# Optimization experiments

Measured on AMD Instinct MI355X. Metric: run time of the kernel, lower is better.

## Reference

```python
import jax, jax.numpy as jnp
import numpy as np

VOCAB_SIZE = 250002
UNUSED_TOKEN_IDS = np.array([0, 2, 1, 3])  # cls, eos, pad, unk (XLM-R tokenizer)
EPS = 1e-12


def _l2norm(x):
    n = jnp.sqrt(jnp.sum(x * x, axis=-1, keepdims=True))
    return x / jnp.maximum(n, EPS)


def setup_inputs() -> dict:
    key = jax.random.key(0)
    k1, k2, k3, k4 = jax.random.split(key, 4)
    B, S, H = 16, 2048, 1024
    hidden_state = jax.random.normal(k1, (B, S, H), dtype=jnp.float32)
    attention_mask = jnp.ones((B, S), dtype=jnp.float32)
    input_ids = jax.random.randint(k2, (B, S), 0, VOCAB_SIZE, dtype=jnp.int64)
    sparse_W = jax.random.normal(k3, (H, 1), dtype=jnp.float32) * 0.02
    sparse_b = jnp.zeros((1,), dtype=jnp.float32)
    colbert_W = jax.random.normal(k4, (H, H), dtype=jnp.float32) * 0.02
    colbert_b = jnp.zeros((H,), dtype=jnp.float32)
    return {
        "hidden_state": hidden_state,
        "attention_mask": attention_mask,
        "input_ids": input_ids,
        "sparse_W": sparse_W,
        "sparse_b": sparse_b,
        "colbert_W": colbert_W,
        "colbert_b": colbert_b,
    }


def reference(hidden_state, attention_mask, input_ids, sparse_W, sparse_b, colbert_W, colbert_b):
    B, S, H = hidden_state.shape
    # dense vector: CLS token, L2-normalized
    dense_vecs = _l2norm(hidden_state[:, 0])  # (B, H)

    # sparse: relu(Linear(H,1)) per token, scatter into vocab, max over seq.
    # scatter into zeros(B,S,V) + max over dim=1 == per-batch scatter-max into (B,V)
    token_weights = jax.nn.relu(
        jnp.einsum("bsh,ho->bso", hidden_state, sparse_W) + sparse_b
    )[..., 0]  # (B, S)
    batch_idx = jnp.arange(B)[:, None]  # (B, 1)
    sparse_vecs = jnp.zeros((B, VOCAB_SIZE), dtype=token_weights.dtype)
    sparse_vecs = sparse_vecs.at[batch_idx, input_ids].max(token_weights)
    # zero out special tokens (cls/eos/pad/unk)
    sparse_vecs = sparse_vecs.at[:, jnp.asarray(UNUSED_TOKEN_IDS)].set(0.0)

    # colbert: Linear(H,H) on tokens 1:, masked, then L2-normalized
    colbert_vecs = jnp.einsum("bsh,hd->bsd", hidden_state[:, 1:], colbert_W) + colbert_b
    colbert_vecs = colbert_vecs * attention_mask[:, 1:, None]
    colbert_vecs = _l2norm(colbert_vecs)  # (B, S-1, H)

    return dense_vecs, sparse_vecs, colbert_vecs
```

## Files before the change

### kernel.cpp

```cpp
#include <hip/hip_runtime.h>
#include <hip/hip_bf16.h>

#define HDIM 1024
#define SEQ  2048
#define BATCH 16
#define VOCAB 250002
#define M_TOT (BATCH * SEQ)
#define DENSE_OFF 0
#define SPARSE_OFF (BATCH * HDIM)
#define COLBERT_OFF (SPARSE_OFF + BATCH * VOCAB)
#define COLBERT_ROWS (BATCH * (SEQ - 1))

typedef __attribute__((ext_vector_type(8))) short short8;
typedef __attribute__((ext_vector_type(4))) float f32x4;

static __device__ __forceinline__ unsigned short f2bf(float f) {
  union { float f; unsigned u; } v; v.f = f;
  unsigned r = v.u + 0x7fffu + ((v.u >> 16) & 1u);
  return (unsigned short)(r >> 16);
}

__global__ __launch_bounds__(256) void cast_sparse_kernel(
    const float* __restrict__ hidden,
    const float* __restrict__ sparse_W,
    const float* __restrict__ sparse_b,
    const int* __restrict__ input_ids,
    unsigned short* __restrict__ hidden_bf,
    float* __restrict__ sparse_out)
{
  const int token = blockIdx.x * 4 + (threadIdx.x >> 6);
  const int lane = threadIdx.x & 63;

  const float4* xr = (const float4*)(hidden + (size_t)token * HDIM);
  const float4* wr = (const float4*)sparse_W;
  ushort4* hb = (ushort4*)(hidden_bf + (size_t)token * HDIM);

  float dot = 0.0f;
#pragma unroll
  for (int i = 0; i < 4; i++) {
    const int idx = i * 64 + lane;
    float4 xv = xr[idx];
    float4 wv = wr[idx];
    dot = fmaf(xv.x, wv.x, dot);
    dot = fmaf(xv.y, wv.y, dot);
    dot = fmaf(xv.z, wv.z, dot);
    dot = fmaf(xv.w, wv.w, dot);
    ushort4 o;
    o.x = f2bf(xv.x); o.y = f2bf(xv.y); o.z = f2bf(xv.z); o.w = f2bf(xv.w);
    hb[idx] = o;
  }
#pragma unroll
  for (int off = 32; off; off >>= 1) dot += __shfl_down(dot, off);

  if (lane == 0) {
    float w = dot + sparse_b[0];
    if (w > 0.0f) {
      int id = input_ids[token];
      if (id > 3) {
        int b = token >> 11;
        atomicMax((int*)(sparse_out + (size_t)b * VOCAB + id), __float_as_int(w));
      }
    }
  }
}

__global__ __launch_bounds__(256) void dense_kernel(
    const float* __restrict__ hidden, float* __restrict__ out)
{
  const int b = blockIdx.x;
  const int t = threadIdx.x;
  const float4* x = (const float4*)(hidden + (size_t)b * SEQ * HDIM);
  float4 v = x[t];
  float ss = v.x * v.x + v.y * v.y + v.z * v.z + v.w * v.w;
#pragma unroll
  for (int off = 32; off; off >>= 1) ss += __shfl_down(ss, off);
  __shared__ float red[4];
  if ((t & 63) == 0) red[t >> 6] = ss;
  __syncthreads();
  float tot = red[0] + red[1] + red[2] + red[3];
  float inv = 1.0f / fmaxf(sqrtf(tot), 1e-12f);
  v.x *= inv; v.y *= inv; v.z *= inv; v.w *= inv;
  ((float4*)(out + (size_t)b * HDIM))[t] = v;
}

__global__ __launch_bounds__(256) void transpose_w_kernel(
    const float* __restrict__ W, unsigned short* __restrict__ Wt)
{
  __shared__ float tile[32][33];
  const int n0 = blockIdx.x * 32, k0 = blockIdx.y * 32;
  const int tx = threadIdx.x, ty = threadIdx.y;
#pragma unroll
  for (int i = ty; i < 32; i += 8)
    tile[i][tx] = W[(size_t)(k0 + i) * HDIM + n0 + tx];
  __syncthreads();
#pragma unroll
  for (int i = ty; i < 32; i += 8)
    Wt[(size_t)(n0 + i) * HDIM + k0 + tx] = f2bf(tile[tx][i]);
}

__global__ __launch_bounds__(256) void gemm_colbert_kernel(
    const unsigned short* __restrict__ Abf,
    const unsigned short* __restrict__ Btbf,
    const float* __restrict__ bias,
    float* __restrict__ out)
{
  __shared__ __attribute__((aligned(16))) unsigned short As[128 * 32];
  __shared__ __attribute__((aligned(16))) unsigned short Bs[128 * 32];

  const int t = threadIdx.x;
  const int wv = t >> 6, l = t & 63;

  const int xcd = blockIdx.x & 7;
  const int local = blockIdx.x >> 3;
  const int mt = xcd * 32 + (local >> 3);
  const int nt = local & 7;
  const int mBase = mt * 128, nBase = nt * 128;
  const int wm = wv >> 1, wn = wv & 1;
  const int q = l >> 4, ml = l & 15;

  f32x4 acc[4][4] = {};

  const int c0 = t;
  const int c1 = t + 256;
  const int r0 = c0 >> 2, r1 = c1 >> 2;
  const size_t ga0 = (size_t)r0 * HDIM + (((c0 & 3) - (r0 >> 1)) & 3) * 8;
  const size_t ga1 = (size_t)r1 * HDIM + (((c1 & 3) - (r1 >> 1)) & 3) * 8;

  const unsigned short* Ab = Abf + (size_t)mBase * HDIM;
  const unsigned short* Bb = Btbf + (size_t)nBase * HDIM;

  for (int k0 = 0; k0 < HDIM; k0 += 32) {
    __builtin_amdgcn_global_load_lds(
        (const __attribute__((address_space(1))) unsigned int*)(Ab + k0 + ga0),
        (__attribute__((address_space(3))) unsigned int*)(As + wv * 512), 16, 0, 0);
    __builtin_amdgcn_global_load_lds(
        (const __attribute__((address_space(1))) unsigned int*)(Ab + k0 + ga1),
        (__attribute__((address_space(3))) unsigned int*)(As + 2048 + wv * 512), 16, 0, 0);
    __builtin_amdgcn_global_load_lds(
        (const __attribute__((address_space(1))) unsigned int*)(Bb + k0 + ga0),
        (__attribute__((address_space(3))) unsigned int*)(Bs + wv * 512), 16, 0, 0);
    __builtin_amdgcn_global_load_lds(
        (const __attribute__((address_space(1))) unsigned int*)(Bb + k0 + ga1),
        (__attribute__((address_space(3))) unsigned int*)(Bs + 2048 + wv * 512), 16, 0, 0);
    __syncthreads();

    short8 af[4], bf[4];
#pragma unroll
    for (int i = 0; i < 4; i++) {
      const int ar = wm * 64 + i * 16 + ml;
      const int br = wn * 64 + i * 16 + ml;
      af[i] = *(const short8*)(As + ar * 32 + (((q + (ar >> 1)) & 3) * 8));
      bf[i] = *(const short8*)(Bs + br * 32 + (((q + (br >> 1)) & 3) * 8));
    }
#pragma unroll
    for (int i = 0; i < 4; i++)
#pragma unroll
      for (int j = 0; j < 4; j++)
        acc[i][j] = __builtin_amdgcn_mfma_f32_16x16x32_bf16(af[i], bf[j], acc[i][j], 0, 0, 0);
    __syncthreads();
  }

#pragma unroll
  for (int j = 0; j < 4; j++) {
    const int gn = nBase + wn * 64 + j * 16 + ml;
    const float bv = bias[gn];
#pragma unroll
    for (int i = 0; i < 4; i++) {
#pragma unroll
      for (int r = 0; r < 4; r++) {
        const int gm = mBase + wm * 64 + i * 16 + q * 4 + r;
        const int s = gm & (SEQ - 1);
        if (s != 0) {
          const int b = gm >> 11;
          out[COLBERT_OFF + (size_t)(b * (SEQ - 1) + s - 1) * HDIM + gn] =
              acc[i][j][r] + bv;
        }
      }
    }
  }
}

__global__ __launch_bounds__(256) void colbert_norm_kernel(
    float* __restrict__ out, const float* __restrict__ mask)
{
  const int row = blockIdx.x * 4 + (threadIdx.x >> 6);
  const int lane = threadIdx.x & 63;
  const int b = row / (SEQ - 1);
  const int s = row - b * (SEQ - 1) + 1;
  const float mval = mask[b * SEQ + s];

  float4* p = (float4*)(out + COLBERT_OFF + (size_t)row * HDIM);
  float4 v[4];
  float ss = 0.0f;
#pragma unroll
  for (int i = 0; i < 4; i++) {
    v[i] = p[i * 64 + lane];
    ss += v[i].x * v[i].x + v[i].y * v[i].y + v[i].z * v[i].z + v[i].w * v[i].w;
  }
#pragma unroll
  for (int off = 32; off; off >>= 1) ss += __shfl_xor(ss, off);
  const float inv = mval / fmaxf(fabsf(mval) * sqrtf(ss), 1e-12f);
#pragma unroll
  for (int i = 0; i < 4; i++) {
    v[i].x *= inv; v[i].y *= inv; v[i].z *= inv; v[i].w *= inv;
    p[i * 64 + lane] = v[i];
  }
}

extern "C" void kernel_launch(void* const* d_in, const int* in_sizes, int n_in,
                              void* d_out, int out_size, void* d_ws, size_t ws_size,
                              hipStream_t stream) {
  (void)in_sizes; (void)n_in; (void)out_size; (void)ws_size;
  const float* hidden = (const float*)d_in[0];
  const float* attn_mask = (const float*)d_in[1];
  const int* input_ids = (const int*)d_in[2];
  const float* sparse_W = (const float*)d_in[3];
  const float* sparse_b = (const float*)d_in[4];
  const float* colbert_W = (const float*)d_in[5];
  const float* colbert_b = (const float*)d_in[6];
  float* out = (float*)d_out;

  unsigned short* hidden_bf = (unsigned short*)d_ws;
  unsigned short* Wt = (unsigned short*)((char*)d_ws + (size_t)M_TOT * HDIM * 2);

  hipMemsetAsync(out + SPARSE_OFF, 0, (size_t)BATCH * VOCAB * sizeof(float), stream);

  cast_sparse_kernel<<<M_TOT / 4, 256, 0, stream>>>(
      hidden, sparse_W, sparse_b, input_ids, hidden_bf, out + SPARSE_OFF);
  transpose_w_kernel<<<dim3(32, 32), dim3(32, 8), 0, stream>>>(colbert_W, Wt);
  dense_kernel<<<BATCH, 256, 0, stream>>>(hidden, out);
  gemm_colbert_kernel<<<(M_TOT / 128) * (HDIM / 128), 256, 0, stream>>>(
      hidden_bf, Wt, colbert_b, out);
  colbert_norm_kernel<<<COLBERT_ROWS / 4, 256, 0, stream>>>(out, attn_mask);
}
```

Measured before the change: 382.5 us.

## Fuse ColBERT L2 norm into GEMM epilogue and merge prep kernels

The GEMM is restructured so each 512-thread block computes 64 full rows across all 1024 output columns. It double-buffers the whole B panel in LDS and computes the row L2 norm, mask and bias in the epilogue before a single write. This removes the separate read-modify-write pass of the colbert output. The memset, the W transpose/cast and the dense CLS normalization are merged into one prep kernel to cut launch count. The cost is a very large dynamic LDS footprint (about 136 KB), which limits occupancy to one block per CU, and every block rereads the full W panel from cache.

Result: no change. 375.6 us (-1.8%).

```diff
diff --git a/kernel.cpp b/kernel.cpp
--- a/kernel.cpp
+++ b/kernel.cpp
@@ -6,10 +6,8 @@
 #define BATCH 16
 #define VOCAB 250002
 #define M_TOT (BATCH * SEQ)
-#define DENSE_OFF 0
 #define SPARSE_OFF (BATCH * HDIM)
 #define COLBERT_OFF (SPARSE_OFF + BATCH * VOCAB)
-#define COLBERT_ROWS (BATCH * (SEQ - 1))
 
 typedef __attribute__((ext_vector_type(8))) short short8;
 typedef __attribute__((ext_vector_type(4))) float f32x4;
@@ -18,6 +16,52 @@
   union { float f; unsigned u; } v; v.f = f;
   unsigned r = v.u + 0x7fffu + ((v.u >> 16) & 1u);
   return (unsigned short)(r >> 16);
+}
+
+static __device__ __forceinline__ void gll16(const unsigned short* g, unsigned short* l) {
+  __builtin_amdgcn_global_load_lds(
+      (const __attribute__((address_space(1))) unsigned int*)g,
+      (__attribute__((address_space(3))) unsigned int*)l, 16, 0, 0);
+}
+
+__global__ __launch_bounds__(256) void prep_kernel(
+    const float* __restrict__ W, unsigned short* __restrict__ Wt,
+    float* __restrict__ out, const float* __restrict__ hidden)
+{
+  __shared__ float tile[32][33];
+  __shared__ float red[4];
+  const int blk = blockIdx.x;
+  if (blk < 1024) {
+    const int n0 = (blk & 31) * 32, k0 = (blk >> 5) * 32;
+    const int tx = threadIdx.x & 31, ty = threadIdx.x >> 5;
+#pragma unroll
+    for (int i = ty; i < 32; i += 8)
+      tile[i][tx] = W[(size_t)(k0 + i) * HDIM + n0 + tx];
+    __syncthreads();
+#pragma unroll
+    for (int i = ty; i < 32; i += 8)
+      Wt[(size_t)(n0 + i) * HDIM + k0 + tx] = f2bf(tile[tx][i]);
+  } else if (blk < 1536) {
+    float4 z = {0.f, 0.f, 0.f, 0.f};
+    float4* p = (float4*)(out + SPARSE_OFF);
+    int idx = (blk - 1024) * 256 + threadIdx.x;
+#pragma unroll 1
+    for (; idx < 1000008; idx += 512 * 256) p[idx] = z;
+  } else {
+    const int b = blk - 1536;
+    const int t = threadIdx.x;
+    const float4* x = (const float4*)(hidden + (size_t)b * SEQ * HDIM);
+    float4 v = x[t];
+    float ss = v.x * v.x + v.y * v.y + v.z * v.z + v.w * v.w;
+#pragma unroll
+    for (int off = 32; off; off >>= 1) ss += __shfl_down(ss, off);
+    if ((t & 63) == 0) red[t >> 6] = ss;
+    __syncthreads();
+    float tot = red[0] + red[1] + red[2] + red[3];
+    float inv = 1.0f / fmaxf(sqrtf(tot), 1e-12f);
+    v.x *= inv; v.y *= inv; v.z *= inv; v.w *= inv;
+    ((float4*)(out + (size_t)b * HDIM))[t] = v;
+  }
 }
 
 __global__ __launch_bounds__(256) void cast_sparse_kernel(
@@ -64,146 +108,144 @@
   }
 }
 
-__global__ __launch_bounds__(256) void dense_kernel(
-    const float* __restrict__ hidden, float* __restrict__ out)
-{
-  const int b = blockIdx.x;
-  const int t = threadIdx.x;
-  const float4* x = (const float4*)(hidden + (size_t)b * SEQ * HDIM);
-  float4 v = x[t];
-  float ss = v.x * v.x + v.y * v.y + v.z * v.z + v.w * v.w;
-#pragma unroll
-  for (int off = 32; off; off >>= 1) ss += __shfl_down(ss, off);
-  __shared__ float red[4];
-  if ((t & 63) == 0) red[t >> 6] = ss;
-  __syncthreads();
-  float tot = red[0] + red[1] + red[2] + red[3];
-  float inv = 1.0f / fmaxf(sqrtf(tot), 1e-12f);
-  v.x *= inv; v.y *= inv; v.z *= inv; v.w *= inv;
-  ((float4*)(out + (size_t)b * HDIM))[t] = v;
-}
-
-__global__ __launch_bounds__(256) void transpose_w_kernel(
-    const float* __restrict__ W, unsigned short* __restrict__ Wt)
-{
-  __shared__ float tile[32][33];
-  const int n0 = blockIdx.x * 32, k0 = blockIdx.y * 32;
-  const int tx = threadIdx.x, ty = threadIdx.y;
-#pragma unroll
-  for (int i = ty; i < 32; i += 8)
-    tile[i][tx] = W[(size_t)(k0 + i) * HDIM + n0 + tx];
-  __syncthreads();
-#pragma unroll
-  for (int i = ty; i < 32; i += 8)
-    Wt[(size_t)(n0 + i) * HDIM + k0 + tx] = f2bf(tile[tx][i]);
-}
-
-__global__ __launch_bounds__(256) void gemm_colbert_kernel(
+#define BS_ELEMS (1024 * 32)
+#define AS_ELEMS (64 * 32)
+#define LDS_BYTES ((2 * BS_ELEMS + 2 * AS_ELEMS) * 2)
+
+__global__ __launch_bounds__(512, 2) void gemm_norm_kernel(
     const unsigned short* __restrict__ Abf,
     const unsigned short* __restrict__ Btbf,
     const float* __restrict__ bias,
+    const float* __restrict__ mask,
     float* __restrict__ out)
 {
-  __shared__ __attribute__((aligned(16))) unsigned short As[128 * 32];
-  __shared__ __attribute__((aligned(16))) unsigned short Bs[128 * 32];
+  extern __shared__ __align__(16) char smem[];
+  unsigned short* Bs0 = (unsigned short*)smem;
+  unsigned short* Bs1 = Bs0 + BS_ELEMS;
+  unsigned short* As0 = Bs1 + BS_ELEMS;
+  unsigned short* As1 = As0 + AS_ELEMS;
+  float* redLDS = (float*)smem;
+  float* invLDS = (float*)smem + 64 * 8;
 
   const int t = threadIdx.x;
   const int wv = t >> 6, l = t & 63;
-
-  const int xcd = blockIdx.x & 7;
-  const int local = blockIdx.x >> 3;
-  const int mt = xcd * 32 + (local >> 3);
-  const int nt = local & 7;
-  const int mBase = mt * 128, nBase = nt * 128;
-  const int wm = wv >> 1, wn = wv & 1;
   const int q = l >> 4, ml = l & 15;
-
-  f32x4 acc[4][4] = {};
-
-  const int c0 = t;
-  const int c1 = t + 256;
-  const int r0 = c0 >> 2, r1 = c1 >> 2;
-  const size_t ga0 = (size_t)r0 * HDIM + (((c0 & 3) - (r0 >> 1)) & 3) * 8;
-  const size_t ga1 = (size_t)r1 * HDIM + (((c1 & 3) - (r1 >> 1)) & 3) * 8;
-
-  const unsigned short* Ab = Abf + (size_t)mBase * HDIM;
-  const unsigned short* Bb = Btbf + (size_t)nBase * HDIM;
-
-  for (int k0 = 0; k0 < HDIM; k0 += 32) {
-    __builtin_amdgcn_global_load_lds(
-        (const __attribute__((address_space(1))) unsigned int*)(Ab + k0 + ga0),
-        (__attribute__((address_space(3))) unsigned int*)(As + wv * 512), 16, 0, 0);
-    __builtin_amdgcn_global_load_lds(
-        (const __attribute__((address_space(1))) unsigned int*)(Ab + k0 + ga1),
-        (__attribute__((address_space(3))) unsigned int*)(As + 2048 + wv * 512), 16, 0, 0);
-    __builtin_amdgcn_global_load_lds(
-        (const __attribute__((address_space(1))) unsigned int*)(Bb + k0 + ga0),
-        (__attribute__((address_space(3))) unsigned int*)(Bs + wv * 512), 16, 0, 0);
-    __builtin_amdgcn_global_load_lds(
-        (const __attribute__((address_space(1))) unsigned int*)(Bb + k0 + ga1),
-        (__attribute__((address_space(3))) unsigned int*)(Bs + 2048 + wv * 512), 16, 0, 0);
+  const int mBase = blockIdx.x * 64;
+
+  int boff[8];
+#pragma unroll
+  for (int c = 0; c < 8; c++) {
+    int cb = c * 512 + wv * 64 + l;
+    int n = cb >> 2;
+    int kc = ((cb & 3) - (n >> 1)) & 3;
+    boff[c] = n * HDIM + kc * 8;
+  }
+  int aoff;
+  {
+    int ca = wv * 64 + l;
+    int row = ca >> 2;
+    int kc = ((ca & 3) - (row >> 1)) & 3;
+    aoff = (mBase + row) * HDIM + kc * 8;
+  }
+
+  f32x4 acc[4][8] = {};
+
+#define STAGE(K0, BD, AD)                                               \
+  do {                                                                  \
+    _Pragma("unroll")                                                   \
+    for (int c = 0; c < 8; c++)                                         \
+      gll16(Btbf + boff[c] + (K0), (BD) + (c * 512 + wv * 64) * 8);     \
+    if (wv < 4) gll16(Abf + aoff + (K0), (AD) + (wv * 64) * 8);         \
+  } while (0)
+
+  STAGE(0, Bs0, As0);
+  __syncthreads();
+
+  for (int kk = 0; kk < 32; kk++) {
+    unsigned short* Bc = (kk & 1) ? Bs1 : Bs0;
+    unsigned short* Ac = (kk & 1) ? As1 : As0;
+    if (kk < 31) {
+      unsigned short* Bn = (kk & 1) ? Bs0 : Bs1;
+      unsigned short* An = (kk & 1) ? As0 : As1;
+      STAGE((kk + 1) * 32, Bn, An);
+    }
+
+    short8 af[4], bf[4];
+#pragma unroll
+    for (int i = 0; i < 4; i++) {
+      const int ar = i * 16 + ml;
+      af[i] = *(const short8*)(Ac + ar * 32 + (((q + (ar >> 1)) & 3) * 8));
+    }
+#pragma unroll
+    for (int jh = 0; jh < 2; jh++) {
+#pragma unroll
+      for (int jj = 0; jj < 4; jj++) {
+        const int br = wv * 128 + (jh * 4 + jj) * 16 + ml;
+        bf[jj] = *(const short8*)(Bc + br * 32 + (((q + (br >> 1)) & 3) * 8));
+      }
+#pragma unroll
+      for (int i = 0; i < 4; i++)
+#pragma unroll
+        for (int jj = 0; jj < 4; jj++)
+          acc[i][jh * 4 + jj] =
+              __builtin_amdgcn_mfma_f32_16x16x32_bf16(af[i], bf[jj], acc[i][jh * 4 + jj], 0, 0, 0);
+    }
     __syncthreads();
-
-    short8 af[4], bf[4];
-#pragma unroll
-    for (int i = 0; i < 4; i++) {
-      const int ar = wm * 64 + i * 16 + ml;
-      const int br = wn * 64 + i * 16 + ml;
-      af[i] = *(const short8*)(As + ar * 32 + (((q + (ar >> 1)) & 3) * 8));
-      bf[i] = *(const short8*)(Bs + br * 32 + (((q + (br >> 1)) & 3) * 8));
-    }
-#pragma unroll
-    for (int i = 0; i < 4; i++)
-#pragma unroll
-      for (int j = 0; j < 4; j++)
-        acc[i][j] = __builtin_amdgcn_mfma_f32_16x16x32_bf16(af[i], bf[j], acc[i][j], 0, 0, 0);
-    __syncthreads();
-  }
-
-#pragma unroll
-  for (int j = 0; j < 4; j++) {
-    const int gn = nBase + wn * 64 + j * 16 + ml;
-    const float bv = bias[gn];
-#pragma unroll
-    for (int i = 0; i < 4; i++) {
-#pragma unroll
-      for (int r = 0; r < 4; r++) {
-        const int gm = mBase + wm * 64 + i * 16 + q * 4 + r;
-        const int s = gm & (SEQ - 1);
-        if (s != 0) {
-          const int b = gm >> 11;
-          out[COLBERT_OFF + (size_t)(b * (SEQ - 1) + s - 1) * HDIM + gn] =
-              acc[i][j][r] + bv;
-        }
+  }
+
+  float bv[8];
+#pragma unroll
+  for (int j = 0; j < 8; j++) bv[j] = bias[wv * 128 + j * 16 + ml];
+#pragma unroll
+  for (int i = 0; i < 4; i++)
+#pragma unroll
+    for (int j = 0; j < 8; j++)
+#pragma unroll
+      for (int r = 0; r < 4; r++) acc[i][j][r] += bv[j];
+
+#pragma unroll
+  for (int i = 0; i < 4; i++) {
+#pragma unroll
+    for (int r = 0; r < 4; r++) {
+      float ss = 0.0f;
+#pragma unroll
+      for (int j = 0; j < 8; j++) { float x = acc[i][j][r]; ss = fmaf(x, x, ss); }
+      ss += __shfl_xor(ss, 1); ss += __shfl_xor(ss, 2);
+      ss += __shfl_xor(ss, 4); ss += __shfl_xor(ss, 8);
+      if (ml == 0) redLDS[(i * 16 + q * 4 + r) * 8 + wv] = ss;
+    }
+  }
+  __syncthreads();
+
+  {
+    const int row = t >> 3, w = t & 7;
+    float v = redLDS[row * 8 + w];
+    v += __shfl_xor(v, 1); v += __shfl_xor(v, 2); v += __shfl_xor(v, 4);
+    if (w == 0) {
+      const int gm = mBase + row;
+      const int s = gm & (SEQ - 1), b = gm >> 11;
+      const float mval = mask[b * SEQ + s];
+      invLDS[row] = mval / fmaxf(fabsf(mval) * sqrtf(v), 1e-12f);
+    }
+  }
+  __syncthreads();
+
+#pragma unroll
+  for (int i = 0; i < 4; i++) {
+#pragma unroll
+    for (int r = 0; r < 4; r++) {
+      const int row = i * 16 + q * 4 + r;
+      const int gm = mBase + row;
+      const int s = gm & (SEQ - 1);
+      if (s != 0) {
+        const int b = gm >> 11;
+        float* orow = out + COLBERT_OFF + (size_t)(b * (SEQ - 1) + s - 1) * HDIM;
+        const float iv = invLDS[row];
+#pragma unroll
+        for (int j = 0; j < 8; j++)
+          orow[wv * 128 + j * 16 + ml] = acc[i][j][r] * iv;
       }
     }
-  }
-}
-
-__global__ __launch_bounds__(256) void colbert_norm_kernel(
-    float* __restrict__ out, const float* __restrict__ mask)
-{
-  const int row = blockIdx.x * 4 + (threadIdx.x >> 6);
-  const int lane = threadIdx.x & 63;
-  const int b = row / (SEQ - 1);
-  const int s = row - b * (SEQ - 1) + 1;
-  const float mval = mask[b * SEQ + s];
-
-  float4* p = (float4*)(out + COLBERT_OFF + (size_t)row * HDIM);
-  float4 v[4];
-  float ss = 0.0f;
-#pragma unroll
-  for (int i = 0; i < 4; i++) {
-    v[i] = p[i * 64 + lane];
-    ss += v[i].x * v[i].x + v[i].y * v[i].y + v[i].z * v[i].z + v[i].w * v[i].w;
-  }
-#pragma unroll
-  for (int off = 32; off; off >>= 1) ss += __shfl_xor(ss, off);
-  const float inv = mval / fmaxf(fabsf(mval) * sqrtf(ss), 1e-12f);
-#pragma unroll
-  for (int i = 0; i < 4; i++) {
-    v[i].x *= inv; v[i].y *= inv; v[i].z *= inv; v[i].w *= inv;
-    p[i * 64 + lane] = v[i];
   }
 }
 
@@ -223,13 +265,9 @@
   unsigned short* hidden_bf = (unsigned short*)d_ws;
   unsigned short* Wt = (unsigned short*)((char*)d_ws + (size_t)M_TOT * HDIM * 2);
 
-  hipMemsetAsync(out + SPARSE_OFF, 0, (size_t)BATCH * VOCAB * sizeof(float), stream);
-
+  prep_kernel<<<1552, 256, 0, stream>>>(colbert_W, Wt, out, hidden);
   cast_sparse_kernel<<<M_TOT / 4, 256, 0, stream>>>(
       hidden, sparse_W, sparse_b, input_ids, hidden_bf, out + SPARSE_OFF);
-  transpose_w_kernel<<<dim3(32, 32), dim3(32, 8), 0, stream>>>(colbert_W, Wt);
-  dense_kernel<<<BATCH, 256, 0, stream>>>(hidden, out);
-  gemm_colbert_kernel<<<(M_TOT / 128) * (HDIM / 128), 256, 0, stream>>>(
-      hidden_bf, Wt, colbert_b, out);
-  colbert_norm_kernel<<<COLBERT_ROWS / 4, 256, 0, stream>>>(out, attn_mask);
-}
+  gemm_norm_kernel<<<M_TOT / 64, 512, LDS_BYTES, stream>>>(
+      hidden_bf, Wt, colbert_b, attn_mask, out);
+}
```
